# Optimization experiments

Measured on AMD Instinct MI355X. Metric: run time of the kernel, lower is better.

The kernel has to match this reference:

```python
import jax, jax.numpy as jnp
import numpy as np

N_NODES = 100000
N_EDGES = 3200000
IN_CH = 24
HIDDEN = 64
N_CLASSES = 16


def _sage_conv(x, src, dst, W_l, b_l, W_r, num_nodes):
    # mean-aggregate neighbor features at destination nodes
    msg = x[src]                                             # [E, F] gather
    agg = jax.ops.segment_sum(msg, dst, num_segments=num_nodes)
    deg = jax.ops.segment_sum(jnp.ones((src.shape[0],), x.dtype), dst,
                              num_segments=num_nodes)
    mean = agg / jnp.maximum(deg, 1.0)[:, None]
    # PyG SAGEConv: lin_l(aggregated) + lin_r(self); bias lives in lin_l
    return mean @ W_l.T + b_l + x @ W_r.T


def setup_inputs() -> dict:
    key = jax.random.key(0)
    ks = jax.random.split(key, 8)
    x = jax.random.normal(ks[0], (N_NODES, IN_CH), dtype=jnp.float32)
    edge_index = jax.random.randint(ks[1], (2, N_EDGES), 0, N_NODES, dtype=jnp.int64)
    s1 = 1.0 / np.sqrt(IN_CH)
    s2 = 1.0 / np.sqrt(HIDDEN)
    return {
        "x": x,
        "edge_index": edge_index,
        "W1_l": jax.random.normal(ks[2], (HIDDEN, IN_CH), dtype=jnp.float32) * s1,
        "b1": jnp.zeros((HIDDEN,), jnp.float32),
        "W1_r": jax.random.normal(ks[3], (HIDDEN, IN_CH), dtype=jnp.float32) * s1,
        "W2_l": jax.random.normal(ks[4], (HIDDEN, HIDDEN), dtype=jnp.float32) * s2,
        "b2": jnp.zeros((HIDDEN,), jnp.float32),
        "W2_r": jax.random.normal(ks[5], (HIDDEN, HIDDEN), dtype=jnp.float32) * s2,
        "Wc": jax.random.normal(ks[6], (N_CLASSES, HIDDEN), dtype=jnp.float32) * s2,
        "bc": jnp.zeros((N_CLASSES,), jnp.float32),
    }


def reference(x, edge_index, W1_l, b1, W1_r, W2_l, b2, W2_r, Wc, bc):
    num_nodes = x.shape[0]
    src, dst = edge_index[0], edge_index[1]
    h = _sage_conv(x, src, dst, W1_l, b1, W1_r, num_nodes)
    h = jax.nn.relu(h)
    # dropout is identity in eval mode
    embeddings = _sage_conv(h, src, dst, W2_l, b2, W2_r, num_nodes)
    logits = embeddings @ Wc.T + bc
    return (logits, embeddings)
```

## Files before the change

### kernel.cpp

```cpp
#include <hip/hip_runtime.h>

#define N_NODES 100000
#define N_EDGES 3200000
#define IN_CH 24
#define HIDDEN 64
#define N_CLASSES 16

#define NBUCK 782
#define CAP 4608
#define PTBLOCKS 256
#define PTCHUNK 12500
#define NCASTB 1563

typedef __attribute__((ext_vector_type(8))) short short8;
typedef __attribute__((ext_vector_type(4))) float float4_;
typedef __attribute__((ext_vector_type(2))) float float2v;
typedef __attribute__((ext_vector_type(4))) int int4v;
typedef __attribute__((ext_vector_type(2))) unsigned uint2v;

__device__ unsigned llvm_amdgcn_raw_buffer_load_u32(int4v, int, int, int) __asm("llvm.amdgcn.raw.buffer.load.i32");
__device__ uint2v llvm_amdgcn_raw_buffer_load_u32x2(int4v, int, int, int) __asm("llvm.amdgcn.raw.buffer.load.v2i32");

__device__ __forceinline__ int4v make_srd(const void* p, unsigned bytes) {
    unsigned long long a = (unsigned long long)p;
    int4v r;
    r.x = (int)(unsigned)a;
    r.y = (int)((unsigned)(a >> 32) & 0xFFFFu);
    r.z = (int)bytes;
    r.w = 0x00020000;
    return r;
}

__device__ __forceinline__ unsigned short f2bf(float f) {
    union { float f; unsigned int u; } v; v.f = f;
    unsigned int u = v.u;
    return (unsigned short)((u + 0x7FFFu + ((u >> 16) & 1u)) >> 16);
}
__device__ __forceinline__ unsigned cvt_pk_bf16(float a, float b) {
    unsigned r;
    asm("v_cvt_pk_bf16_f32 %0, %1, %2" : "=v"(r) : "v"(a), "v"(b));
    return r;
}
__device__ __forceinline__ unsigned short pk_fp8(float a, float b) {
    return (unsigned short)(__builtin_amdgcn_cvt_pk_fp8_f32(a, b, 0, false) & 0xFFFF);
}
__device__ __forceinline__ void accum_dw(float2v* A, unsigned w) {
    A[0] += __builtin_amdgcn_cvt_pk_f32_fp8(w, false);
    A[1] += __builtin_amdgcn_cvt_pk_f32_fp8(w, true);
}
__device__ __forceinline__ short8 mk8(unsigned d0, unsigned d1, unsigned d2, unsigned d3) {
    union { unsigned u[4]; short8 s; } v;
    v.u[0] = d0; v.u[1] = d1; v.u[2] = d2; v.u[3] = d3;
    return v.s;
}


__global__ __launch_bounds__(1024) void k_partx(const int* __restrict__ src,
                                                const int* __restrict__ dst,
                                                int* __restrict__ bucketFill,
                                                unsigned int* __restrict__ pedges,
                                                const float* __restrict__ x,
                                                unsigned short* __restrict__ X8s,
                                                const float* __restrict__ W1l,
                                                const float* __restrict__ W1r,
                                                const float* __restrict__ W2l,
                                                const float* __restrict__ W2r,
                                                const float* __restrict__ Wc,
                                                const float* __restrict__ b2,
                                                const float* __restrict__ bc,
                                                unsigned short* __restrict__ Bt1,
                                                unsigned short* __restrict__ Bt2,
                                                float* __restrict__ bias2) {
    __shared__ int cntL[NBUCK];
    __shared__ int baseL[NBUCK];
    int t = threadIdx.x;
    int bid = blockIdx.x;
    if (bid >= PTBLOCKS) {
        if (bid < PTBLOCKS + NCASTB) {
            int gid = (bid - PTBLOCKS) * 1024 + t;
            if (gid >= N_NODES * 16) return;
            int n = gid >> 4, kp = gid & 15;
            if (kp < 12) {
                const float2 v = *(const float2*)(x + n * 24 + kp * 2);
                X8s[n * 16 + kp] = pk_fp8(v.x, v.y);
            } else {
                X8s[n * 16 + kp] = 0;
            }
        } else {
            for (int i = t; i < 64 * 64; i += 1024) {
                int o = i >> 6, k = i & 63;
                float v = (k < 24) ? W1r[o * 24 + k]
                                   : ((k < 48) ? W1l[o * 24 + k - 24] : 0.f);
                Bt1[i] = f2bf(v);
            }
            for (int i = t; i < 64 * 128; i += 1024) {
                int o = i >> 7, k = i & 127;
                float v = (k < 64) ? W2l[o * 64 + k] : W2r[o * 64 + k - 64];
                Bt2[i] = f2bf(v);
            }
            for (int i = t; i < 16 * 128; i += 1024) {
                int c = i >> 7, k = i & 127;
                const float* M = (k < 64) ? W2l : W2r;
                int kk = k & 63;
                float s = 0.f;
                for (int j = 0; j < 64; j++) s += Wc[c * 64 + j] * M[j * 64 + kk];
                Bt2[(64 + c) * 128 + k] = f2bf(s);
            }
            for (int i = t; i < 80; i += 1024) {
                if (i < 64) bias2[i] = b2[i];
                else {
                    int c = i - 64;
                    float s = bc[c];
                    for (int j = 0; j < 64; j++) s += Wc[c * 64 + j] * b2[j];
                    bias2[i] = s;
                }
            }
        }
        return;
    }
    int cbeg = bid * PTCHUNK;
    int d[13], s[13];
#pragma unroll
    for (int k = 0; k < 13; k++) {
        int o = k * 1024 + t;
        bool ok = o < PTCHUNK;
        d[k] = ok ? dst[cbeg + o] : -1;
        s[k] = ok ? src[cbeg + o] : 0;
    }
    for (int i = t; i < NBUCK; i += 1024) cntL[i] = 0;
    __syncthreads();
#pragma unroll
    for (int k = 0; k < 13; k++)
        if (d[k] >= 0) atomicAdd(&cntL[d[k] >> 7], 1);
    __syncthreads();
    for (int i = t; i < NBUCK; i += 1024) {
        int c = cntL[i];
        if (c) baseL[i] = i * CAP + atomicAdd(&bucketFill[i], c);
        cntL[i] = 0;
    }
    __syncthreads();
#pragma unroll
    for (int k = 0; k < 13; k++)
        if (d[k] >= 0) {
            int bk = d[k] >> 7;
            int r = atomicAdd(&cntL[bk], 1);
            pedges[baseL[bk] + r] = ((unsigned int)(d[k] & 127) << 17) | (unsigned int)s[k];
        }
}

__global__ __launch_bounds__(1024) void k_bucket(const unsigned int* __restrict__ pedges,
                                                 const int* __restrict__ bucketFill,
                                                 int2* __restrict__ begend,
                                                 int* __restrict__ srcs, int N) {
    __shared__ int ncnt[128];
    __shared__ int sps[128];
    int b = blockIdx.x;
    int t = threadIdx.x;
    int eb0 = b * CAP;
    int m = bucketFill[b];
    unsigned int v[5];
#pragma unroll
    for (int k = 0; k < 5; k++) {
        int o = k * 1024 + t;
        v[k] = (o < m) ? pedges[eb0 + o] : 0xFFFFFFFFu;
    }
    if (t < 128) ncnt[t] = 0;
    __syncthreads();
#pragma unroll
    for (int k = 0; k < 5; k++)
        if (v[k] != 0xFFFFFFFFu) atomicAdd(&ncnt[v[k] >> 17], 1);
    __syncthreads();
    int myc = (t < 128) ? ncnt[t] : 0;
    int val = myc;
    if (t < 128) sps[t] = val;
    __syncthreads();
    for (int off = 1; off < 128; off <<= 1) {
        int vv = (t >= off && t < 128) ? sps[t - off] : 0;
        __syncthreads();
        if (t < 128) { val += vv; sps[t] = val; }
        __syncthreads();
    }
    int mybase = val - myc;
    int node = b * 128 + t;
    if (t < 128 && node < N) {
        int2 be; be.x = eb0 + mybase; be.y = eb0 + mybase + myc;
        begend[node] = be;
    }
    if (t < 128) { sps[t] = mybase; ncnt[t] = 0; }
    if (t < 32) srcs[eb0 + m + t] = 0;
    __syncthreads();
#pragma unroll
    for (int k = 0; k < 5; k++)
        if (v[k] != 0xFFFFFFFFu) {
            unsigned int nl = v[k] >> 17;
            int r = atomicAdd(&ncnt[nl], 1);
            srcs[eb0 + sps[nl] + r] = (int)(v[k] & 0x1FFFF);
        }
}


__global__ __launch_bounds__(1024) void k_fuse1(const float* __restrict__ x,
                                                const unsigned int* __restrict__ X8u,
                                                const int2* __restrict__ begend,
                                                const int* __restrict__ srcs,
                                                const unsigned short* __restrict__ Bt1,
                                                const float* __restrict__ b1,
                                                unsigned short* __restrict__ A2s,
                                                unsigned char* __restrict__ H8b) {
    __shared__ unsigned int lds_mean[16][20];
    int w = threadIdx.x >> 6;
    int lane = threadIdx.x & 63;
    int base = blockIdx.x * 16;
    int grp = lane >> 3;
    int sub = lane & 7;
    const int4v srdX = make_srd(X8u, N_NODES * 32u);
    const int4v srdS = make_srd(srcs, (unsigned)NBUCK * CAP * 4u);
    int suboff = sub * 4;

    {
        int2 be = begend[base + w];
        int b = be.x, e = be.y;
        float2v A[2] = {{0.f, 0.f}, {0.f, 0.f}};
        int nfull = (e - b) & ~31;
        int j = b;
        int vo = (b + grp) * 4;
        for (; j < b + nfull; j += 32, vo += 128) {
            int s0 = (int)llvm_amdgcn_raw_buffer_load_u32(srdS, vo, 0, 0);
            int s1 = (int)llvm_amdgcn_raw_buffer_load_u32(srdS, vo + 32, 0, 0);
            int s2 = (int)llvm_amdgcn_raw_buffer_load_u32(srdS, vo + 64, 0, 0);
            int s3 = (int)llvm_amdgcn_raw_buffer_load_u32(srdS, vo + 96, 0, 0);
            unsigned u0 = llvm_amdgcn_raw_buffer_load_u32(srdX, (s0 << 5) + suboff, 0, 0);
            unsigned u1 = llvm_amdgcn_raw_buffer_load_u32(srdX, (s1 << 5) + suboff, 0, 0);
            unsigned u2 = llvm_amdgcn_raw_buffer_load_u32(srdX, (s2 << 5) + suboff, 0, 0);
            unsigned u3 = llvm_amdgcn_raw_buffer_load_u32(srdX, (s3 << 5) + suboff, 0, 0);
            accum_dw(A, u0); accum_dw(A, u1); accum_dw(A, u2); accum_dw(A, u3);
        }
        if (j < e) {
            int j0 = j + grp;
            int s0 = (int)llvm_amdgcn_raw_buffer_load_u32(srdS, vo, 0, 0);
            int s1 = (int)llvm_amdgcn_raw_buffer_load_u32(srdS, vo + 32, 0, 0);
            int s2 = (int)llvm_amdgcn_raw_buffer_load_u32(srdS, vo + 64, 0, 0);
            int s3 = (int)llvm_amdgcn_raw_buffer_load_u32(srdS, vo + 96, 0, 0);
            int o0 = (j0 < e)      ? ((s0 << 5) + suboff) : 0x7FFF0000;
            int o1 = (j0 + 8 < e)  ? ((s1 << 5) + suboff) : 0x7FFF0000;
            int o2 = (j0 + 16 < e) ? ((s2 << 5) + suboff) : 0x7FFF0000;
            int o3 = (j0 + 24 < e) ? ((s3 << 5) + suboff) : 0x7FFF0000;
            unsigned u0 = llvm_amdgcn_raw_buffer_load_u32(srdX, o0, 0, 0);
            unsigned u1 = llvm_amdgcn_raw_buffer_load_u32(srdX, o1, 0, 0);
            unsigned u2 = llvm_amdgcn_raw_buffer_load_u32(srdX, o2, 0, 0);
            unsigned u3 = llvm_amdgcn_raw_buffer_load_u32(srdX, o3, 0, 0);
            accum_dw(A, u0); accum_dw(A, u1); accum_dw(A, u2); accum_dw(A, u3);
        }
#pragma unroll
        for (int mm = 8; mm <= 32; mm <<= 1) {
#pragma unroll
            for (int q = 0; q < 2; q++) {
                float2v t;
                t.x = __shfl_xor(A[q].x, mm, 64);
                t.y = __shfl_xor(A[q].y, mm, 64);
                A[q] += t;
            }
        }
        if (lane < 8) {
            float inv = __builtin_amdgcn_rcpf((float)max(e - b, 1));
            lds_mean[w][sub * 2]     = cvt_pk_bf16(A[0].x * inv, A[0].y * inv);
            lds_mean[w][sub * 2 + 1] = cvt_pk_bf16(A[1].x * inv, A[1].y * inv);
        }
    }
    __syncthreads();
    if (w >= 4) return;

    int m = lane & 15, quad = lane >> 4;
    int row = base + m;
    short8 bf0 = *(const short8*)(Bt1 + (w * 16 + m) * 64 + quad * 8);
    short8 bf1 = *(const short8*)(Bt1 + (w * 16 + m) * 64 + 32 + quad * 8);
    float bias = b1[w * 16 + m];
    short8 a0, a1;
    if (quad < 3) {
        const float4* xp = (const float4*)(x + row * 24 + quad * 8);
        float4 v0 = xp[0], v1 = xp[1];
        a0 = mk8(cvt_pk_bf16(v0.x, v0.y), cvt_pk_bf16(v0.z, v0.w),
                 cvt_pk_bf16(v1.x, v1.y), cvt_pk_bf16(v1.z, v1.w));
    } else {
        a0 = *(const short8*)&lds_mean[m][0];
    }
    if (quad == 0)      a1 = *(const short8*)&lds_mean[m][4];
    else if (quad == 1) a1 = *(const short8*)&lds_mean[m][8];
    else                a1 = mk8(0u, 0u, 0u, 0u);
    float4_ c = {0.f, 0.f, 0.f, 0.f};
    c = __builtin_amdgcn_mfma_f32_16x16x32_bf16(a0, bf0, c, 0, 0, 0);
    c = __builtin_amdgcn_mfma_f32_16x16x32_bf16(a1, bf1, c, 0, 0, 0);
    int col = w * 16 + m;
#pragma unroll
    for (int r = 0; r < 4; r++) {
        int row2 = base + quad * 4 + r;
        float v = fmaxf(c[r] + bias, 0.f);
        A2s[row2 * 128 + 64 + col] = f2bf(v);
        H8b[row2 * 64 + col] =
            (unsigned char)(__builtin_amdgcn_cvt_pk_fp8_f32(v, 0.f, 0, false) & 0xFF);
    }
}

__global__ __launch_bounds__(1024) void k_fuse2(const unsigned int* __restrict__ H8u,
                                                const int2* __restrict__ begend,
                                                const int* __restrict__ srcs,
                                                const unsigned short* __restrict__ Bt2,
                                                const float* __restrict__ bias2,
                                                unsigned short* A2s,
                                                float* __restrict__ logits) {
    __shared__ unsigned int lds_h[16][36];
    int w = threadIdx.x >> 6;
    int lane = threadIdx.x & 63;
    int base = blockIdx.x * 16;
    int grp = lane >> 3;
    int sub = lane & 7;
    const int4v srdH = make_srd(H8u, N_NODES * 64u);
    const int4v srdS = make_srd(srcs, (unsigned)NBUCK * CAP * 4u);
    int suboff = sub * 8;

    {
        int2 be = begend[base + w];
        int b = be.x, e = be.y;
        float2v A[4] = {{0.f, 0.f}, {0.f, 0.f}, {0.f, 0.f}, {0.f, 0.f}};
        int nfull = (e - b) & ~31;
        int j = b;
        int vo = (b + grp) * 4;
        for (; j < b + nfull; j += 32, vo += 128) {
            int s0 = (int)llvm_amdgcn_raw_buffer_load_u32(srdS, vo, 0, 0);
            int s1 = (int)llvm_amdgcn_raw_buffer_load_u32(srdS, vo + 32, 0, 0);
            int s2 = (int)llvm_amdgcn_raw_buffer_load_u32(srdS, vo + 64, 0, 0);
            int s3 = (int)llvm_amdgcn_raw_buffer_load_u32(srdS, vo + 96, 0, 0);
            uint2v u0 = llvm_amdgcn_raw_buffer_load_u32x2(srdH, (s0 << 6) + suboff, 0, 0);
            uint2v u1 = llvm_amdgcn_raw_buffer_load_u32x2(srdH, (s1 << 6) + suboff, 0, 0);
            uint2v u2 = llvm_amdgcn_raw_buffer_load_u32x2(srdH, (s2 << 6) + suboff, 0, 0);
            uint2v u3 = llvm_amdgcn_raw_buffer_load_u32x2(srdH, (s3 << 6) + suboff, 0, 0);
            accum_dw(A, u0.x); accum_dw(A + 2, u0.y);
            accum_dw(A, u1.x); accum_dw(A + 2, u1.y);
            accum_dw(A, u2.x); accum_dw(A + 2, u2.y);
            accum_dw(A, u3.x); accum_dw(A + 2, u3.y);
        }
        if (j < e) {
            int j0 = j + grp;
            int s0 = (int)llvm_amdgcn_raw_buffer_load_u32(srdS, vo, 0, 0);
            int s1 = (int)llvm_amdgcn_raw_buffer_load_u32(srdS, vo + 32, 0, 0);
            int s2 = (int)llvm_amdgcn_raw_buffer_load_u32(srdS, vo + 64, 0, 0);
            int s3 = (int)llvm_amdgcn_raw_buffer_load_u32(srdS, vo + 96, 0, 0);
            int o0 = (j0 < e)      ? ((s0 << 6) + suboff) : 0x7FFF0000;
            int o1 = (j0 + 8 < e)  ? ((s1 << 6) + suboff) : 0x7FFF0000;
            int o2 = (j0 + 16 < e) ? ((s2 << 6) + suboff) : 0x7FFF0000;
            int o3 = (j0 + 24 < e) ? ((s3 << 6) + suboff) : 0x7FFF0000;
            uint2v u0 = llvm_amdgcn_raw_buffer_load_u32x2(srdH, o0, 0, 0);
            uint2v u1 = llvm_amdgcn_raw_buffer_load_u32x2(srdH, o1, 0, 0);
            uint2v u2 = llvm_amdgcn_raw_buffer_load_u32x2(srdH, o2, 0, 0);
            uint2v u3 = llvm_amdgcn_raw_buffer_load_u32x2(srdH, o3, 0, 0);
            accum_dw(A, u0.x); accum_dw(A + 2, u0.y);
            accum_dw(A, u1.x); accum_dw(A + 2, u1.y);
            accum_dw(A, u2.x); accum_dw(A + 2, u2.y);
            accum_dw(A, u3.x); accum_dw(A + 2, u3.y);
        }
#pragma unroll
        for (int mm = 8; mm <= 32; mm <<= 1) {
#pragma unroll
            for (int q = 0; q < 4; q++) {
                float2v t;
                t.x = __shfl_xor(A[q].x, mm, 64);
                t.y = __shfl_xor(A[q].y, mm, 64);
                A[q] += t;
            }
        }
        if (lane < 8) {
            float inv = __builtin_amdgcn_rcpf((float)max(e - b, 1));
            uint4 o;
            o.x = cvt_pk_bf16(A[0].x * inv, A[0].y * inv);
            o.y = cvt_pk_bf16(A[1].x * inv, A[1].y * inv);
            o.z = cvt_pk_bf16(A[2].x * inv, A[2].y * inv);
            o.w = cvt_pk_bf16(A[3].x * inv, A[3].y * inv);
            *(uint4*)&lds_h[w][sub * 4] = o;
        }
    }
    __syncthreads();

    int m = lane & 15, quad = lane >> 4;
    int row = base + m;
    short8 a2, a3, bf[4];
    float bias = 0.f;
    bool doP2 = (w < 5);
    if (doP2) {
        int trow = ((w < 4) ? w * 16 : 64) + m;
#pragma unroll
        for (int s = 0; s < 4; s++)
            bf[s] = *(const short8*)(Bt2 + trow * 128 + s * 32 + quad * 8);
        bias = bias2[trow];
        a2 = *(const short8*)(A2s + row * 128 + 64 + quad * 8);
        a3 = *(const short8*)(A2s + row * 128 + 96 + quad * 8);
    }
    __syncthreads();
    if (!doP2) return;
    short8 a0 = *(const short8*)&lds_h[m][quad * 4];
    short8 a1 = *(const short8*)&lds_h[m][16 + quad * 4];
    float4_ c = {0.f, 0.f, 0.f, 0.f};
    c = __builtin_amdgcn_mfma_f32_16x16x32_bf16(a0, bf[0], c, 0, 0, 0);
    c = __builtin_amdgcn_mfma_f32_16x16x32_bf16(a1, bf[1], c, 0, 0, 0);
    c = __builtin_amdgcn_mfma_f32_16x16x32_bf16(a2, bf[2], c, 0, 0, 0);
    c = __builtin_amdgcn_mfma_f32_16x16x32_bf16(a3, bf[3], c, 0, 0, 0);
    if (w < 4) {
        float* embp = (float*)A2s;
        int col = w * 16 + m;
#pragma unroll
        for (int r = 0; r < 4; r++) {
            int row2 = base + quad * 4 + r;
            embp[row2 * 64 + col] = c[r] + bias;
        }
    } else {
#pragma unroll
        for (int r = 0; r < 4; r++) {
            int row2 = base + quad * 4 + r;
            logits[row2 * 16 + m] = c[r] + bias;
        }
    }
}


extern "C" void kernel_launch(void* const* d_in, const int* in_sizes, int n_in,
                              void* d_out, int out_size, void* d_ws, size_t ws_size,
                              hipStream_t stream) {
    const float* x = (const float*)d_in[0];
    const int* edge = (const int*)d_in[1];
    const int* srcIdx = edge;
    const int* dstIdx = edge + N_EDGES;
    const float* W1l = (const float*)d_in[2];
    const float* b1  = (const float*)d_in[3];
    const float* W1r = (const float*)d_in[4];
    const float* W2l = (const float*)d_in[5];
    const float* b2  = (const float*)d_in[6];
    const float* W2r = (const float*)d_in[7];
    const float* Wc  = (const float*)d_in[8];
    const float* bc  = (const float*)d_in[9];

    float* logits = (float*)d_out;
    unsigned short* A2s = (unsigned short*)((float*)d_out + (size_t)N_NODES * N_CLASSES);

    char* w = (char*)d_ws;
    auto carve = [&](size_t bytes) {
        char* p = w;
        w += (bytes + 255) & ~(size_t)255;
        return p;
    };
    int2* begend         = (int2*)carve((size_t)N_NODES * sizeof(int2));
    int* srcs            = (int*)carve((size_t)NBUCK * CAP * sizeof(int));
    unsigned int* pedges = (unsigned int*)carve((size_t)NBUCK * CAP * sizeof(unsigned int));
    unsigned short* X8s  = (unsigned short*)carve((size_t)N_NODES * 32);
    unsigned char* H8b   = (unsigned char*)carve((size_t)N_NODES * 64);
    int* bucketFill      = (int*)carve(NBUCK * sizeof(int));
    unsigned short* Bt1  = (unsigned short*)carve(64 * 64 * sizeof(unsigned short));
    unsigned short* Bt2  = (unsigned short*)carve(80 * 128 * sizeof(unsigned short));
    float* bias2         = (float*)carve(80 * sizeof(float));

    unsigned int* X8u = (unsigned int*)X8s;
    unsigned int* H8u = (unsigned int*)H8b;

    hipMemsetAsync(bucketFill, 0, NBUCK * sizeof(int), stream);
    k_partx<<<PTBLOCKS + NCASTB + 1, 1024, 0, stream>>>(
        srcIdx, dstIdx, bucketFill, pedges, x, X8s,
        W1l, W1r, W2l, W2r, Wc, b2, bc, Bt1, Bt2, bias2);
    k_bucket<<<NBUCK, 1024, 0, stream>>>(pedges, bucketFill, begend, srcs, N_NODES);

    int fgrid = N_NODES / 16;
    k_fuse1<<<fgrid, 1024, 0, stream>>>(x, X8u, begend, srcs, Bt1, b1, A2s, H8b);
    k_fuse2<<<fgrid, 1024, 0, stream>>>(H8u, begend, srcs, Bt2, bias2, A2s, logits);
}
```

Before: 272.5 us.

## Shrink fused SAGE blocks to two waves, each aggregating eight nodes

Both fused aggregation+GEMM kernels move from 16 waves per block (one wave per destination node) to 2 waves per block, each wave looping over 8 nodes serially. The MFMA epilogue is redistributed so each of the two waves computes two or three 16-column output tiles instead of idle waves returning early. This aims to cut block-level barrier overhead and idle waves in the GEMM phase and improve scheduling granularity. In exchange each wave's gather work is serialized over 8 nodes, reducing memory-level parallelism per wave unless occupancy compensates.

```diff
diff --git a/kernel.cpp b/kernel.cpp
--- a/kernel.cpp
+++ b/kernel.cpp
@@ -199,14 +199,14 @@
 }
 
 
-__global__ __launch_bounds__(1024) void k_fuse1(const float* __restrict__ x,
-                                                const unsigned int* __restrict__ X8u,
-                                                const int2* __restrict__ begend,
-                                                const int* __restrict__ srcs,
-                                                const unsigned short* __restrict__ Bt1,
-                                                const float* __restrict__ b1,
-                                                unsigned short* __restrict__ A2s,
-                                                unsigned char* __restrict__ H8b) {
+__global__ __launch_bounds__(128) void k_fuse1(const float* __restrict__ x,
+                                               const unsigned int* __restrict__ X8u,
+                                               const int2* __restrict__ begend,
+                                               const int* __restrict__ srcs,
+                                               const unsigned short* __restrict__ Bt1,
+                                               const float* __restrict__ b1,
+                                               unsigned short* __restrict__ A2s,
+                                               unsigned char* __restrict__ H8b) {
     __shared__ unsigned int lds_mean[16][20];
     int w = threadIdx.x >> 6;
     int lane = threadIdx.x & 63;
@@ -217,8 +217,9 @@
     const int4v srdS = make_srd(srcs, (unsigned)NBUCK * CAP * 4u);
     int suboff = sub * 4;
 
-    {
-        int2 be = begend[base + w];
+    for (int i = 0; i < 8; i++) {
+        int il = w * 8 + i;
+        int2 be = begend[base + il];
         int b = be.x, e = be.y;
         float2v A[2] = {{0.f, 0.f}, {0.f, 0.f}};
         int nfull = (e - b) & ~31;
@@ -263,18 +264,14 @@
         }
         if (lane < 8) {
             float inv = __builtin_amdgcn_rcpf((float)max(e - b, 1));
-            lds_mean[w][sub * 2]     = cvt_pk_bf16(A[0].x * inv, A[0].y * inv);
-            lds_mean[w][sub * 2 + 1] = cvt_pk_bf16(A[1].x * inv, A[1].y * inv);
-        }
-    }
-    __syncthreads();
-    if (w >= 4) return;
+            lds_mean[il][sub * 2]     = cvt_pk_bf16(A[0].x * inv, A[0].y * inv);
+            lds_mean[il][sub * 2 + 1] = cvt_pk_bf16(A[1].x * inv, A[1].y * inv);
+        }
+    }
+    __syncthreads();
 
     int m = lane & 15, quad = lane >> 4;
     int row = base + m;
-    short8 bf0 = *(const short8*)(Bt1 + (w * 16 + m) * 64 + quad * 8);
-    short8 bf1 = *(const short8*)(Bt1 + (w * 16 + m) * 64 + 32 + quad * 8);
-    float bias = b1[w * 16 + m];
     short8 a0, a1;
     if (quad < 3) {
         const float4* xp = (const float4*)(x + row * 24 + quad * 8);
@@ -287,27 +284,34 @@
     if (quad == 0)      a1 = *(const short8*)&lds_mean[m][4];
     else if (quad == 1) a1 = *(const short8*)&lds_mean[m][8];
     else                a1 = mk8(0u, 0u, 0u, 0u);
-    float4_ c = {0.f, 0.f, 0.f, 0.f};
-    c = __builtin_amdgcn_mfma_f32_16x16x32_bf16(a0, bf0, c, 0, 0, 0);
-    c = __builtin_amdgcn_mfma_f32_16x16x32_bf16(a1, bf1, c, 0, 0, 0);
-    int col = w * 16 + m;
-#pragma unroll
-    for (int r = 0; r < 4; r++) {
-        int row2 = base + quad * 4 + r;
-        float v = fmaxf(c[r] + bias, 0.f);
-        A2s[row2 * 128 + 64 + col] = f2bf(v);
-        H8b[row2 * 64 + col] =
-            (unsigned char)(__builtin_amdgcn_cvt_pk_fp8_f32(v, 0.f, 0, false) & 0xFF);
-    }
-}
-
-__global__ __launch_bounds__(1024) void k_fuse2(const unsigned int* __restrict__ H8u,
-                                                const int2* __restrict__ begend,
-                                                const int* __restrict__ srcs,
-                                                const unsigned short* __restrict__ Bt2,
-                                                const float* __restrict__ bias2,
-                                                unsigned short* A2s,
-                                                float* __restrict__ logits) {
+#pragma unroll
+    for (int tt = 0; tt < 2; tt++) {
+        int t = w * 2 + tt;
+        short8 bf0 = *(const short8*)(Bt1 + (t * 16 + m) * 64 + quad * 8);
+        short8 bf1 = *(const short8*)(Bt1 + (t * 16 + m) * 64 + 32 + quad * 8);
+        float bias = b1[t * 16 + m];
+        float4_ c = {0.f, 0.f, 0.f, 0.f};
+        c = __builtin_amdgcn_mfma_f32_16x16x32_bf16(a0, bf0, c, 0, 0, 0);
+        c = __builtin_amdgcn_mfma_f32_16x16x32_bf16(a1, bf1, c, 0, 0, 0);
+        int col = t * 16 + m;
+#pragma unroll
+        for (int r = 0; r < 4; r++) {
+            int row2 = base + quad * 4 + r;
+            float v = fmaxf(c[r] + bias, 0.f);
+            A2s[row2 * 128 + 64 + col] = f2bf(v);
+            H8b[row2 * 64 + col] =
+                (unsigned char)(__builtin_amdgcn_cvt_pk_fp8_f32(v, 0.f, 0, false) & 0xFF);
+        }
+    }
+}
+
+__global__ __launch_bounds__(128) void k_fuse2(const unsigned int* __restrict__ H8u,
+                                               const int2* __restrict__ begend,
+                                               const int* __restrict__ srcs,
+                                               const unsigned short* __restrict__ Bt2,
+                                               const float* __restrict__ bias2,
+                                               unsigned short* A2s,
+                                               float* __restrict__ logits) {
     __shared__ unsigned int lds_h[16][36];
     int w = threadIdx.x >> 6;
     int lane = threadIdx.x & 63;
@@ -318,8 +322,9 @@
     const int4v srdS = make_srd(srcs, (unsigned)NBUCK * CAP * 4u);
     int suboff = sub * 8;
 
-    {
-        int2 be = begend[base + w];
+    for (int i = 0; i < 8; i++) {
+        int il = w * 8 + i;
+        int2 be = begend[base + il];
         int b = be.x, e = be.y;
         float2v A[4] = {{0.f, 0.f}, {0.f, 0.f}, {0.f, 0.f}, {0.f, 0.f}};
         int nfull = (e - b) & ~31;
@@ -375,47 +380,48 @@
             o.y = cvt_pk_bf16(A[1].x * inv, A[1].y * inv);
             o.z = cvt_pk_bf16(A[2].x * inv, A[2].y * inv);
             o.w = cvt_pk_bf16(A[3].x * inv, A[3].y * inv);
-            *(uint4*)&lds_h[w][sub * 4] = o;
+            *(uint4*)&lds_h[il][sub * 4] = o;
         }
     }
     __syncthreads();
 
     int m = lane & 15, quad = lane >> 4;
     int row = base + m;
-    short8 a2, a3, bf[4];
-    float bias = 0.f;
-    bool doP2 = (w < 5);
-    if (doP2) {
-        int trow = ((w < 4) ? w * 16 : 64) + m;
-#pragma unroll
-        for (int s = 0; s < 4; s++)
-            bf[s] = *(const short8*)(Bt2 + trow * 128 + s * 32 + quad * 8);
-        bias = bias2[trow];
-        a2 = *(const short8*)(A2s + row * 128 + 64 + quad * 8);
-        a3 = *(const short8*)(A2s + row * 128 + 96 + quad * 8);
-    }
-    __syncthreads();
-    if (!doP2) return;
+    short8 a2 = *(const short8*)(A2s + row * 128 + 64 + quad * 8);
+    short8 a3 = *(const short8*)(A2s + row * 128 + 96 + quad * 8);
+    __syncthreads();
     short8 a0 = *(const short8*)&lds_h[m][quad * 4];
     short8 a1 = *(const short8*)&lds_h[m][16 + quad * 4];
-    float4_ c = {0.f, 0.f, 0.f, 0.f};
-    c = __builtin_amdgcn_mfma_f32_16x16x32_bf16(a0, bf[0], c, 0, 0, 0);
-    c = __builtin_amdgcn_mfma_f32_16x16x32_bf16(a1, bf[1], c, 0, 0, 0);
-    c = __builtin_amdgcn_mfma_f32_16x16x32_bf16(a2, bf[2], c, 0, 0, 0);
-    c = __builtin_amdgcn_mfma_f32_16x16x32_bf16(a3, bf[3], c, 0, 0, 0);
-    if (w < 4) {
-        float* embp = (float*)A2s;
-        int col = w * 16 + m;
-#pragma unroll
-        for (int r = 0; r < 4; r++) {
-            int row2 = base + quad * 4 + r;
-            embp[row2 * 64 + col] = c[r] + bias;
-        }
-    } else {
-#pragma unroll
-        for (int r = 0; r < 4; r++) {
-            int row2 = base + quad * 4 + r;
-            logits[row2 * 16 + m] = c[r] + bias;
+    int ntile = (w == 0) ? 2 : 3;
+#pragma unroll
+    for (int tt = 0; tt < 3; tt++) {
+        if (tt >= ntile) break;
+        int t = (w == 0) ? tt : 2 + tt;
+        int trow = ((t < 4) ? t * 16 : 64) + m;
+        short8 bf0 = *(const short8*)(Bt2 + trow * 128 + quad * 8);
+        short8 bf1 = *(const short8*)(Bt2 + trow * 128 + 32 + quad * 8);
+        short8 bf2 = *(const short8*)(Bt2 + trow * 128 + 64 + quad * 8);
+        short8 bf3 = *(const short8*)(Bt2 + trow * 128 + 96 + quad * 8);
+        float bias = bias2[trow];
+        float4_ c = {0.f, 0.f, 0.f, 0.f};
+        c = __builtin_amdgcn_mfma_f32_16x16x32_bf16(a0, bf0, c, 0, 0, 0);
+        c = __builtin_amdgcn_mfma_f32_16x16x32_bf16(a1, bf1, c, 0, 0, 0);
+        c = __builtin_amdgcn_mfma_f32_16x16x32_bf16(a2, bf2, c, 0, 0, 0);
+        c = __builtin_amdgcn_mfma_f32_16x16x32_bf16(a3, bf3, c, 0, 0, 0);
+        if (t < 4) {
+            float* embp = (float*)A2s;
+            int col = t * 16 + m;
+#pragma unroll
+            for (int r = 0; r < 4; r++) {
+                int row2 = base + quad * 4 + r;
+                embp[row2 * 64 + col] = c[r] + bias;
+            }
+        } else {
+#pragma unroll
+            for (int r = 0; r < 4; r++) {
+                int row2 = base + quad * 4 + r;
+                logits[row2 * 16 + m] = c[r] + bias;
+            }
         }
     }
 }
@@ -466,6 +472,6 @@
     k_bucket<<<NBUCK, 1024, 0, stream>>>(pedges, bucketFill, begend, srcs, N_NODES);
 
     int fgrid = N_NODES / 16;
-    k_fuse1<<<fgrid, 1024, 0, stream>>>(x, X8u, begend, srcs, Bt1, b1, A2s, H8b);
-    k_fuse2<<<fgrid, 1024, 0, stream>>>(H8u, begend, srcs, Bt2, bias2, A2s, logits);
-}
+    k_fuse1<<<fgrid, 128, 0, stream>>>(x, X8u, begend, srcs, Bt1, b1, A2s, H8b);
+    k_fuse2<<<fgrid, 128, 0, stream>>>(H8u, begend, srcs, Bt2, bias2, A2s, logits);
+}
```

Result: faster. 247.7 us (median of 2 runs) (-9.1%).
